# Kernel optimization log

Hardware: AMD Instinct MI355X
Metric: run time of the kernel (lower is better)

## Reference

```python
import jax, jax.numpy as jnp
import numpy as np

TEMPERATURE = 0.1
NEG_INF = -1e30  # finite sentinel to keep logsumexp grad-safe


def setup_inputs() -> dict:
    key = jax.random.key(0)
    k_emb, k_lab = jax.random.split(key)
    B, D, C = 8192, 256, 100
    embeddings = jax.random.normal(k_emb, (B, D), dtype=jnp.float32)
    labels = jax.random.randint(k_lab, (B,), 0, C, dtype=jnp.int64)
    return {"embeddings": embeddings, "labels": labels}


def reference(embeddings, labels):
    B = embeddings.shape[0]
    # squared L2 pairwise distance: ||x_i||^2 + ||x_j||^2 - 2 x_i . x_j
    sq = jnp.sum(embeddings * embeddings, axis=1)  # [B]
    gram = jnp.einsum('id,jd->ij', embeddings, embeddings)  # [B,B]
    dist2 = jnp.maximum(sq[:, None] + sq[None, :] - 2.0 * gram, 0.0)
    sim = -dist2 / TEMPERATURE  # [B,B]

    same = labels[:, None] == labels[None, :]
    eye = jnp.eye(B, dtype=bool)
    pos_mask = same & ~eye
    neg_mask = ~same

    # per-row uniform random positive via Gumbel-argmax over pos_mask
    k_sel = jax.random.key(42)
    g = jax.random.gumbel(k_sel, (B, B), dtype=jnp.float32)
    j = jnp.argmax(jnp.where(pos_mask, g, -jnp.inf), axis=1)  # [B]

    numerator = jnp.take_along_axis(sim, j[:, None], axis=1)[:, 0]  # sim[i, j_i]
    denominator = jax.nn.logsumexp(jnp.where(neg_mask, sim, NEG_INF), axis=1)

    valid = pos_mask.any(axis=1) & neg_mask.any(axis=1)
    per_row = -(numerator - denominator)
    n_valid = jnp.sum(valid)
    loss = jnp.sum(jnp.where(valid, per_row, 0.0)) / jnp.maximum(n_valid, 1)
    return jnp.where(n_valid > 0, loss, 0.0)
```

## Files before the change

### kernel.cpp

```cpp
#include <hip/hip_runtime.h>
#include <float.h>
#include <math.h>


#define B_N 8192
#define D_K 256
#define NCLS 100
#define MAXC 512
#define NSPLIT 16
#define NPART NSPLIT
#define JR (B_N / NSPLIT)
#define BI 128
#define BJ 64
#define NJT (JR / BJ)
#define BK 64
#define NKC (D_K / BK)
#define NEG_INF -1e30f
#define C2F  (-14.426950408889634f)
#define K2A  (28.853900817779268f)
#define LN2F (0.6931471805599453f)

typedef __attribute__((ext_vector_type(8))) short bf16x8;
typedef __attribute__((ext_vector_type(4))) float f32x4;
typedef unsigned short ushort_t;

__device__ __forceinline__ float ex2(float x){ return __builtin_amdgcn_exp2f(x); }
__device__ __forceinline__ float lg2(float x){ return __builtin_amdgcn_logf(x); }

__device__ __forceinline__ unsigned rotl32(unsigned x, int d){ return (x << d) | (x >> (32 - d)); }

__device__ __forceinline__ float gumbel_at(unsigned idx){
  const unsigned HALF = (unsigned)B_N * (unsigned)B_N / 2u;
  unsigned c0, c1; bool second;
  if (idx < HALF){ c0 = idx; c1 = idx + HALF; second = false; }
  else            { c0 = idx - HALF; c1 = idx; second = true; }
  const unsigned ks0 = 0u, ks1 = 42u, ks2 = 0u ^ 42u ^ 0x1BD11BDAu;
  unsigned x0 = c0 + ks0, x1 = c1 + ks1;
#define TF_RND(r) { x0 += x1; x1 = rotl32(x1, (r)); x1 ^= x0; }
  TF_RND(13) TF_RND(15) TF_RND(26) TF_RND(6)   x0 += ks1; x1 += ks2 + 1u;
  TF_RND(17) TF_RND(29) TF_RND(16) TF_RND(24)  x0 += ks2; x1 += ks0 + 2u;
  TF_RND(13) TF_RND(15) TF_RND(26) TF_RND(6)   x0 += ks0; x1 += ks1 + 3u;
  TF_RND(17) TF_RND(29) TF_RND(16) TF_RND(24)  x0 += ks1; x1 += ks2 + 4u;
  TF_RND(13) TF_RND(15) TF_RND(26) TF_RND(6)   x0 += ks2; x1 += ks0 + 5u;
#undef TF_RND
  unsigned bits = second ? x1 : x0;
  float u = __uint_as_float((bits >> 9) | 0x3f800000u) - 1.0f;
  const float TINY = 1.17549435e-38f;
  u = u * (1.0f - TINY) + TINY;
  u = fmaxf(TINY, u);
  return -logf(-logf(u));
}

__device__ __forceinline__ ushort_t f2bf(float x){
  unsigned u = __float_as_uint(x);
  return (ushort_t)((u + 0x7FFFu + ((u >> 16) & 1u)) >> 16);
}

__device__ __forceinline__ void async16(const ushort_t* g, ushort_t* lds_wave_base){
  __builtin_amdgcn_global_load_lds((const __attribute__((address_space(1))) void*)g,
                                   (__attribute__((address_space(3))) void*)lds_wave_base,
                                   16, 0, 0);
}

__global__ __launch_bounds__(256)
void prep_kernel(const float* __restrict__ E, ushort_t* __restrict__ Ebf,
                 float* __restrict__ sq, float* __restrict__ acc4,
                 const int* __restrict__ labels, int* __restrict__ cls_cnt,
                 int* __restrict__ clist){
  __shared__ int s_list[MAXC];
  __shared__ int s_n;
  if (blockIdx.x < B_N / 4){
    if (blockIdx.x == 0 && threadIdx.x < 4) acc4[threadIdx.x] = 0.f;
    int w = threadIdx.x >> 6, lane = threadIdx.x & 63;
    int row = blockIdx.x * 4 + w;
    const float4 v = *reinterpret_cast<const float4*>(E + (size_t)row * D_K + lane * 4);
    float s = v.x*v.x + v.y*v.y + v.z*v.z + v.w*v.w;
#pragma unroll
    for (int off = 32; off > 0; off >>= 1) s += __shfl_down(s, off);
    if (lane == 0) sq[row] = s;
    ushort4 o; o.x = f2bf(v.x); o.y = f2bf(v.y); o.z = f2bf(v.z); o.w = f2bf(v.w);
    *reinterpret_cast<ushort4*>(Ebf + (size_t)row * D_K + lane * 4) = o;
  } else {
    const int c = blockIdx.x - B_N / 4;
    const int tid = threadIdx.x;
    if (tid == 0) s_n = 0;
    __syncthreads();
    for (int t = tid; t < B_N; t += 256){
      if (labels[t] == c){
        int p = atomicAdd(&s_n, 1);
        if (p < MAXC) s_list[p] = t;
      }
    }
    __syncthreads();
    const int n = min(s_n, MAXC);
    if (tid == 0) cls_cnt[c] = n;
    for (int t = tid; t < n; t += 256) clist[c * MAXC + t] = s_list[t];
  }
}

__global__ __launch_bounds__(256)
void rowsel_kernel(const int* __restrict__ labels, const int* __restrict__ cls_cnt,
                   const int* __restrict__ clist, int* __restrict__ jsel){
  const int w = threadIdx.x >> 6, lane = threadIdx.x & 63;
  const int row = blockIdx.x * 4 + w;
  const int c = labels[row];
  const int n = min(cls_cnt[c], MAXC);
  float gb = -FLT_MAX; int jb = -1;
  for (int t = lane; t < n; t += 64){
    int j = clist[c * MAXC + t];
    if (j != row){
      float g = gumbel_at(((unsigned)row << 13) + (unsigned)j);
      if (g > gb || (g == gb && (unsigned)j < (unsigned)jb)){ gb = g; jb = j; }
    }
  }
#pragma unroll
  for (int off = 32; off > 0; off >>= 1){
    float g2 = __shfl_down(gb, off);
    int   j2 = __shfl_down(jb, off);
    if (g2 > gb || (g2 == gb && (unsigned)j2 < (unsigned)jb)){ gb = g2; jb = j2; }
  }
  if (lane == 0) jsel[row] = jb;
}

__global__ __launch_bounds__(256, 3)
void fused_kernel(const ushort_t* __restrict__ Ebf, const int* __restrict__ labels,
                  const float* __restrict__ sq, const int* __restrict__ jsel,
                  float* __restrict__ numer,
                  float* __restrict__ wsM, float* __restrict__ wsS)
{
  __shared__ __align__(16) ushort_t Bs[2][BJ * BK];
  __shared__ float s_h2j[JR];
  __shared__ int   s_lj[JR];
  __shared__ float s_h2i[BI];
  __shared__ int   s_li[BI];
  __shared__ int   s_ji[BI];

  const int bi    = blockIdx.x >> 4;
  const int split = blockIdx.x & 15;
  const int i0    = bi * BI;
  const int jbase = split * JR;
  const int tid   = threadIdx.x;
  const int lane  = tid & 63;
  const int w     = tid >> 6;
  const int quad  = lane >> 4;
  const int l15   = lane & 15;

  for (int t = tid; t < JR; t += 256){ s_h2j[t] = C2F * sq[jbase + t]; s_lj[t] = labels[jbase + t]; }
  if (tid < BI){ s_h2i[tid] = C2F * sq[i0 + tid]; s_li[tid] = labels[i0 + tid]; s_ji[tid] = jsel[i0 + tid]; }

  bf16x8 af[2][8];
#pragma unroll
  for (int mt = 0; mt < 2; mt++){
    const ushort_t* rp = Ebf + (size_t)(i0 + w * 32 + mt * 16 + l15) * D_K + quad * 8;
#pragma unroll
    for (int c = 0; c < 8; c++)
      af[mt][c] = *reinterpret_cast<const bf16x8*>(rp + c * 32);
  }

  f32x4 acc[2][4];
#pragma unroll
  for (int mt = 0; mt < 2; mt++)
#pragma unroll
    for (int nt = 0; nt < 4; nt++) acc[mt][nt] = (f32x4)0.f;
  float sm[8], ssum[8];
#pragma unroll
  for (int r = 0; r < 8; r++){ sm[r] = NEG_INF; ssum[r] = 0.f; }

  int soff[2];
#pragma unroll
  for (int rd = 0; rd < 2; rd++){
    int slot = rd * 256 + tid;
    int r = slot >> 3, gs = slot & 7;
    soff[rd] = r * D_K + ((gs ^ (r & 7)) << 3);
  }

#pragma unroll
  for (int rd = 0; rd < 2; rd++)
    async16(Ebf + (size_t)jbase * D_K + soff[rd],
            &Bs[0][(size_t)(rd * 256 + w * 64) * 8]);
  __syncthreads();

#pragma unroll 1
  for (int jt = 0; jt < NJT; jt++){
    const int j0 = jbase + jt * BJ;
#pragma unroll
    for (int kc = 0; kc < NKC; kc++){
      const int b = kc & 1;
      const int sn = jt * NKC + kc + 1;
      if (sn < NJT * NKC){
        const int kcn = sn & 3;
        const size_t gb0 = (size_t)(jbase + (sn >> 2) * BJ) * D_K + (size_t)kcn * BK;
#pragma unroll
        for (int rd = 0; rd < 2; rd++)
          async16(Ebf + gb0 + soff[rd],
                  &Bs[b ^ 1][(size_t)(rd * 256 + w * 64) * 8]);
      }
#pragma unroll
      for (int s = 0; s < 2; s++){
        const int g = s * 4 + quad;
        const int c = kc * 2 + s;
        bf16x8 bfr[4];
#pragma unroll
        for (int q = 0; q < 4; q++){
          int r = q * 16 + l15;
          bfr[q] = *reinterpret_cast<const bf16x8*>(&Bs[b][r * BK + ((g ^ (r & 7)) << 3)]);
        }
#pragma unroll
        for (int q = 0; q < 4; q++){
          acc[0][q] = __builtin_amdgcn_mfma_f32_16x16x32_bf16(af[0][c], bfr[q], acc[0][q], 0, 0, 0);
          acc[1][q] = __builtin_amdgcn_mfma_f32_16x16x32_bf16(af[1][c], bfr[q], acc[1][q], 0, 0, 0);
        }
      }
      if (kc == NKC - 1){
        float h2j[4]; int lj[4];
#pragma unroll
        for (int nt = 0; nt < 4; nt++){
          int ccol = jt * BJ + nt * 16 + l15;
          h2j[nt] = s_h2j[ccol]; lj[nt] = s_lj[ccol];
        }
#pragma unroll
        for (int mt = 0; mt < 2; mt++){
#pragma unroll
          for (int rr = 0; rr < 4; rr++){
            const int rl = w * 32 + mt * 16 + quad * 4 + rr;
            const float h2i = s_h2i[rl];
            const int lrow = s_li[rl], jsl = s_ji[rl];
            float sv[4];
#pragma unroll
            for (int nt = 0; nt < 4; nt++){
              float a = acc[mt][nt][rr];
              float sim2 = fminf(fmaf(K2A, a, h2i + h2j[nt]), 0.f);
              int colg = j0 + nt * 16 + l15;
              if (colg == jsl) numer[i0 + rl] = sim2;
              sv[nt] = (lj[nt] != lrow) ? sim2 : NEG_INF;
            }
            float m4 = fmaxf(fmaxf(sv[0], sv[1]), fmaxf(sv[2], sv[3]));
            float s4 = ex2(sv[0]-m4)+ex2(sv[1]-m4)+ex2(sv[2]-m4)+ex2(sv[3]-m4);
            const int sidx = mt * 4 + rr;
            float M = fmaxf(sm[sidx], m4);
            ssum[sidx] = ssum[sidx]*ex2(sm[sidx]-M) + s4*ex2(m4-M);
            sm[sidx] = M;
          }
        }
#pragma unroll
        for (int mt = 0; mt < 2; mt++)
#pragma unroll
          for (int nt = 0; nt < 4; nt++) acc[mt][nt] = (f32x4)0.f;
      }
      __syncthreads();
    }
  }

#pragma unroll
  for (int sidx = 0; sidx < 8; sidx++){
    float mv = sm[sidx], sv2 = ssum[sidx];
#pragma unroll
    for (int mask = 1; mask < 16; mask <<= 1){
      float m2 = __shfl_xor(mv, mask);
      float s2 = __shfl_xor(sv2, mask);
      float M = fmaxf(mv, m2);
      sv2 = sv2 * ex2(mv - M) + s2 * ex2(m2 - M);
      mv = M;
    }
    if (l15 == 0){
      const int mt = sidx >> 2, rr = sidx & 3;
      int rl = w * 32 + mt * 16 + quad * 4 + rr;
      int o = split * B_N + i0 + rl;
      wsM[o] = mv; wsS[o] = sv2;
    }
  }
}

__global__ __launch_bounds__(256)
void finale_kernel(const float* __restrict__ wsM, const float* __restrict__ wsS,
                   const float* __restrict__ numer, const int* __restrict__ jsel,
                   float* __restrict__ acc4, float* __restrict__ out)
{
  const int tid = threadIdx.x;
  const int row = blockIdx.x * 256 + tid;
  float M = -3.0e38f, S = 0.f;
#pragma unroll
  for (int p = 0; p < NPART; p++){
    float m2 = wsM[p * B_N + row], s2 = wsS[p * B_N + row];
    float Mn = fmaxf(M, m2);
    S = S * ex2(M - Mn) + s2 * ex2(m2 - Mn);
    M = Mn;
  }
  bool v = (jsel[row] >= 0) && (M > -5e29f);
  float s = v ? (LN2F * (M + lg2(S) - numer[row])) : 0.f;
  unsigned n = v ? 1u : 0u;
#pragma unroll
  for (int off = 32; off > 0; off >>= 1){ s += __shfl_down(s, off); n += __shfl_down(n, off); }
  __shared__ float ssm[4]; __shared__ unsigned snm[4];
  if ((tid & 63) == 0){ ssm[tid >> 6] = s; snm[tid >> 6] = n; }
  __syncthreads();
  if (tid == 0){
    float bs = ssm[0] + ssm[1] + ssm[2] + ssm[3];
    unsigned bn = snm[0] + snm[1] + snm[2] + snm[3];
    atomicAdd(&acc4[0], bs);
    atomicAdd((unsigned*)&acc4[1], bn);
    __threadfence();
    unsigned old = atomicAdd((unsigned*)&acc4[2], 1u);
    if (old == 31u){
      float St = atomicAdd(&acc4[0], 0.f);
      unsigned Nt = atomicAdd((unsigned*)&acc4[1], 0u);
      out[0] = (Nt > 0u) ? (St / (float)Nt) : 0.f;
    }
  }
}

extern "C" void kernel_launch(void* const* d_in, const int* in_sizes, int n_in,
                              void* d_out, int out_size, void* d_ws, size_t ws_size,
                              hipStream_t stream)
{
  const float* E      = (const float*)d_in[0];
  const int*   labels = (const int*)d_in[1];
  float*       out    = (float*)d_out;

  ushort_t* Ebf = (ushort_t*)d_ws;
  float* wsM    = (float*)(Ebf + (size_t)B_N * D_K);
  float* wsS    = wsM + NPART * B_N;
  float* sqb    = wsS + NPART * B_N;
  float* numer  = sqb + B_N;
  int* jsel     = (int*)(numer + B_N);
  float* acc4   = (float*)(jsel + B_N);
  int* cls_cnt  = (int*)(acc4 + 4);
  int* clist    = cls_cnt + NCLS;

  prep_kernel<<<B_N / 4 + NCLS, 256, 0, stream>>>(E, Ebf, sqb, acc4, labels, cls_cnt, clist);
  rowsel_kernel<<<B_N / 4, 256, 0, stream>>>(labels, cls_cnt, clist, jsel);
  fused_kernel<<<(B_N / BI) * NSPLIT, 256, 0, stream>>>(Ebf, labels, sqb, jsel, numer, wsM, wsS);
  finale_kernel<<<B_N / 256, 256, 0, stream>>>(wsM, wsS, numer, jsel, acc4, out);
}
```

Before: 145.5 us.

## Deepen LDS prefetch ring and fold positive selection into prep kernel

```diff
diff --git a/kernel.cpp b/kernel.cpp
--- a/kernel.cpp
+++ b/kernel.cpp
@@ -15,6 +15,8 @@
 #define NJT (JR / BJ)
 #define BK 64
 #define NKC (D_K / BK)
+#define NSTEP (NJT * NKC)
+#define TOTB ((B_N / BI) * NSPLIT)
 #define NEG_INF -1e30f
 #define C2F  (-14.426950408889634f)
 #define K2A  (28.853900817779268f)
@@ -65,8 +67,7 @@
 __global__ __launch_bounds__(256)
 void prep_kernel(const float* __restrict__ E, ushort_t* __restrict__ Ebf,
                  float* __restrict__ sq, float* __restrict__ acc4,
-                 const int* __restrict__ labels, int* __restrict__ cls_cnt,
-                 int* __restrict__ clist){
+                 const int* __restrict__ labels, int* __restrict__ jsel){
   __shared__ int s_list[MAXC];
   __shared__ int s_n;
   if (blockIdx.x < B_N / 4){
@@ -83,6 +84,7 @@
   } else {
     const int c = blockIdx.x - B_N / 4;
     const int tid = threadIdx.x;
+    const int w = tid >> 6, lane = tid & 63;
     if (tid == 0) s_n = 0;
     __syncthreads();
     for (int t = tid; t < B_N; t += 256){
@@ -93,42 +95,34 @@
     }
     __syncthreads();
     const int n = min(s_n, MAXC);
-    if (tid == 0) cls_cnt[c] = n;
-    for (int t = tid; t < n; t += 256) clist[c * MAXC + t] = s_list[t];
+    for (int m = w; m < n; m += 4){
+      const int row = s_list[m];
+      float gb = -FLT_MAX; int jb = -1;
+      for (int t = lane; t < n; t += 64){
+        int j = s_list[t];
+        if (j != row){
+          float g = gumbel_at(((unsigned)row << 13) + (unsigned)j);
+          if (g > gb || (g == gb && (unsigned)j < (unsigned)jb)){ gb = g; jb = j; }
+        }
+      }
+#pragma unroll
+      for (int off = 32; off > 0; off >>= 1){
+        float g2 = __shfl_down(gb, off);
+        int   j2 = __shfl_down(jb, off);
+        if (g2 > gb || (g2 == gb && (unsigned)j2 < (unsigned)jb)){ gb = g2; jb = j2; }
+      }
+      if (lane == 0) jsel[row] = jb;
+    }
   }
 }
 
 __global__ __launch_bounds__(256)
-void rowsel_kernel(const int* __restrict__ labels, const int* __restrict__ cls_cnt,
-                   const int* __restrict__ clist, int* __restrict__ jsel){
-  const int w = threadIdx.x >> 6, lane = threadIdx.x & 63;
-  const int row = blockIdx.x * 4 + w;
-  const int c = labels[row];
-  const int n = min(cls_cnt[c], MAXC);
-  float gb = -FLT_MAX; int jb = -1;
-  for (int t = lane; t < n; t += 64){
-    int j = clist[c * MAXC + t];
-    if (j != row){
-      float g = gumbel_at(((unsigned)row << 13) + (unsigned)j);
-      if (g > gb || (g == gb && (unsigned)j < (unsigned)jb)){ gb = g; jb = j; }
-    }
-  }
-#pragma unroll
-  for (int off = 32; off > 0; off >>= 1){
-    float g2 = __shfl_down(gb, off);
-    int   j2 = __shfl_down(jb, off);
-    if (g2 > gb || (g2 == gb && (unsigned)j2 < (unsigned)jb)){ gb = g2; jb = j2; }
-  }
-  if (lane == 0) jsel[row] = jb;
-}
-
-__global__ __launch_bounds__(256, 3)
 void fused_kernel(const ushort_t* __restrict__ Ebf, const int* __restrict__ labels,
                   const float* __restrict__ sq, const int* __restrict__ jsel,
                   float* __restrict__ numer,
                   float* __restrict__ wsM, float* __restrict__ wsS)
 {
-  __shared__ __align__(16) ushort_t Bs[2][BJ * BK];
+  __shared__ __align__(16) ushort_t Bs[4][BJ * BK];
   __shared__ float s_h2j[JR];
   __shared__ int   s_lj[JR];
   __shared__ float s_h2i[BI];
@@ -148,24 +142,6 @@
   for (int t = tid; t < JR; t += 256){ s_h2j[t] = C2F * sq[jbase + t]; s_lj[t] = labels[jbase + t]; }
   if (tid < BI){ s_h2i[tid] = C2F * sq[i0 + tid]; s_li[tid] = labels[i0 + tid]; s_ji[tid] = jsel[i0 + tid]; }
 
-  bf16x8 af[2][8];
-#pragma unroll
-  for (int mt = 0; mt < 2; mt++){
-    const ushort_t* rp = Ebf + (size_t)(i0 + w * 32 + mt * 16 + l15) * D_K + quad * 8;
-#pragma unroll
-    for (int c = 0; c < 8; c++)
-      af[mt][c] = *reinterpret_cast<const bf16x8*>(rp + c * 32);
-  }
-
-  f32x4 acc[2][4];
-#pragma unroll
-  for (int mt = 0; mt < 2; mt++)
-#pragma unroll
-    for (int nt = 0; nt < 4; nt++) acc[mt][nt] = (f32x4)0.f;
-  float sm[8], ssum[8];
-#pragma unroll
-  for (int r = 0; r < 8; r++){ sm[r] = NEG_INF; ssum[r] = 0.f; }
-
   int soff[2];
 #pragma unroll
   for (int rd = 0; rd < 2; rd++){
@@ -175,9 +151,30 @@
   }
 
 #pragma unroll
-  for (int rd = 0; rd < 2; rd++)
-    async16(Ebf + (size_t)jbase * D_K + soff[rd],
-            &Bs[0][(size_t)(rd * 256 + w * 64) * 8]);
+  for (int st = 0; st < 2; st++)
+#pragma unroll
+    for (int rd = 0; rd < 2; rd++)
+      async16(Ebf + (size_t)jbase * D_K + (size_t)st * BK + soff[rd],
+              &Bs[st][(size_t)(rd * 256 + w * 64) * 8]);
+
+  bf16x8 af[2][8];
+#pragma unroll
+  for (int mt = 0; mt < 2; mt++){
+    const ushort_t* rp = Ebf + (size_t)(i0 + w * 32 + mt * 16 + l15) * D_K + quad * 8;
+#pragma unroll
+    for (int c = 0; c < 8; c++)
+      af[mt][c] = *reinterpret_cast<const bf16x8*>(rp + c * 32);
+  }
+
+  f32x4 acc[2][4];
+#pragma unroll
+  for (int mt = 0; mt < 2; mt++)
+#pragma unroll
+    for (int nt = 0; nt < 4; nt++) acc[mt][nt] = (f32x4)0.f;
+  float sm[8], ssum[8];
+#pragma unroll
+  for (int r = 0; r < 8; r++){ sm[r] = NEG_INF; ssum[r] = 0.f; }
+
   __syncthreads();
 
 #pragma unroll 1
@@ -185,32 +182,33 @@
     const int j0 = jbase + jt * BJ;
 #pragma unroll
     for (int kc = 0; kc < NKC; kc++){
-      const int b = kc & 1;
-      const int sn = jt * NKC + kc + 1;
-      if (sn < NJT * NKC){
-        const int kcn = sn & 3;
-        const size_t gb0 = (size_t)(jbase + (sn >> 2) * BJ) * D_K + (size_t)kcn * BK;
+      const int st = jt * NKC + kc;
+      if (st <= NSTEP - 3){
+        const int sn = st + 2;
+        const size_t gb0 = (size_t)(jbase + (sn >> 2) * BJ) * D_K + (size_t)(sn & 3) * BK;
 #pragma unroll
         for (int rd = 0; rd < 2; rd++)
-          async16(Ebf + gb0 + soff[rd],
-                  &Bs[b ^ 1][(size_t)(rd * 256 + w * 64) * 8]);
-      }
+          async16(Ebf + gb0 + soff[rd], &Bs[sn & 3][(size_t)(rd * 256 + w * 64) * 8]);
+        asm volatile("s_waitcnt vmcnt(4)\n\ts_barrier" ::: "memory");
+      } else if (st == NSTEP - 2){
+        asm volatile("s_waitcnt vmcnt(2)\n\ts_barrier" ::: "memory");
+      } else {
+        asm volatile("s_waitcnt vmcnt(0)\n\ts_barrier" ::: "memory");
+      }
+      __builtin_amdgcn_s_setprio(1);
 #pragma unroll
       for (int s = 0; s < 2; s++){
         const int g = s * 4 + quad;
         const int c = kc * 2 + s;
-        bf16x8 bfr[4];
 #pragma unroll
         for (int q = 0; q < 4; q++){
-          int r = q * 16 + l15;
-          bfr[q] = *reinterpret_cast<const bf16x8*>(&Bs[b][r * BK + ((g ^ (r & 7)) << 3)]);
+          const int r = q * 16 + l15;
+          bf16x8 bq = *reinterpret_cast<const bf16x8*>(&Bs[kc][r * BK + ((g ^ (r & 7)) << 3)]);
+          acc[0][q] = __builtin_amdgcn_mfma_f32_16x16x32_bf16(af[0][c], bq, acc[0][q], 0, 0, 0);
+          acc[1][q] = __builtin_amdgcn_mfma_f32_16x16x32_bf16(af[1][c], bq, acc[1][q], 0, 0, 0);
         }
-#pragma unroll
-        for (int q = 0; q < 4; q++){
-          acc[0][q] = __builtin_amdgcn_mfma_f32_16x16x32_bf16(af[0][c], bfr[q], acc[0][q], 0, 0, 0);
-          acc[1][q] = __builtin_amdgcn_mfma_f32_16x16x32_bf16(af[1][c], bfr[q], acc[1][q], 0, 0, 0);
-        }
-      }
+      }
+      __builtin_amdgcn_s_setprio(0);
       if (kc == NKC - 1){
         float h2j[4]; int lj[4];
 #pragma unroll
@@ -247,7 +245,6 @@
 #pragma unroll
           for (int nt = 0; nt < 4; nt++) acc[mt][nt] = (f32x4)0.f;
       }
-      __syncthreads();
     }
   }
 
@@ -324,11 +321,8 @@
   float* numer  = sqb + B_N;
   int* jsel     = (int*)(numer + B_N);
   float* acc4   = (float*)(jsel + B_N);
-  int* cls_cnt  = (int*)(acc4 + 4);
-  int* clist    = cls_cnt + NCLS;
-
-  prep_kernel<<<B_N / 4 + NCLS, 256, 0, stream>>>(E, Ebf, sqb, acc4, labels, cls_cnt, clist);
-  rowsel_kernel<<<B_N / 4, 256, 0, stream>>>(labels, cls_cnt, clist, jsel);
-  fused_kernel<<<(B_N / BI) * NSPLIT, 256, 0, stream>>>(Ebf, labels, sqb, jsel, numer, wsM, wsS);
+
+  prep_kernel<<<B_N / 4 + NCLS, 256, 0, stream>>>(E, Ebf, sqb, acc4, labels, jsel);
+  fused_kernel<<<TOTB, 256, 0, stream>>>(Ebf, labels, sqb, jsel, numer, wsM, wsS);
   finale_kernel<<<B_N / 256, 256, 0, stream>>>(wsM, wsS, numer, jsel, acc4, out);
 }
```

New measurement: 179.8 us. 1.24x slower.

## Load full-K B tile per j-tile instead of double-buffered K chunks

Applied to the files above, without the earlier changes.

```diff
diff --git a/kernel.cpp b/kernel.cpp
--- a/kernel.cpp
+++ b/kernel.cpp
@@ -13,8 +13,7 @@
 #define BI 128
 #define BJ 64
 #define NJT (JR / BJ)
-#define BK 64
-#define NKC (D_K / BK)
+#define TOTB ((B_N / BI) * NSPLIT)
 #define NEG_INF -1e30f
 #define C2F  (-14.426950408889634f)
 #define K2A  (28.853900817779268f)
@@ -122,13 +121,13 @@
   if (lane == 0) jsel[row] = jb;
 }
 
-__global__ __launch_bounds__(256, 3)
+__global__ __launch_bounds__(256)
 void fused_kernel(const ushort_t* __restrict__ Ebf, const int* __restrict__ labels,
                   const float* __restrict__ sq, const int* __restrict__ jsel,
                   float* __restrict__ numer,
                   float* __restrict__ wsM, float* __restrict__ wsS)
 {
-  __shared__ __align__(16) ushort_t Bs[2][BJ * BK];
+  __shared__ __align__(16) ushort_t Bs[BJ * D_K];
   __shared__ float s_h2j[JR];
   __shared__ int   s_lj[JR];
   __shared__ float s_h2i[BI];
@@ -166,89 +165,74 @@
 #pragma unroll
   for (int r = 0; r < 8; r++){ sm[r] = NEG_INF; ssum[r] = 0.f; }
 
-  int soff[2];
-#pragma unroll
-  for (int rd = 0; rd < 2; rd++){
-    int slot = rd * 256 + tid;
-    int r = slot >> 3, gs = slot & 7;
-    soff[rd] = r * D_K + ((gs ^ (r & 7)) << 3);
-  }
-
-#pragma unroll
-  for (int rd = 0; rd < 2; rd++)
-    async16(Ebf + (size_t)jbase * D_K + soff[rd],
-            &Bs[0][(size_t)(rd * 256 + w * 64) * 8]);
+  const int soff0 = (tid >> 5) * D_K + (((tid & 31) ^ ((tid >> 5) & 7)) << 3);
+
   __syncthreads();
 
 #pragma unroll 1
   for (int jt = 0; jt < NJT; jt++){
     const int j0 = jbase + jt * BJ;
-#pragma unroll
-    for (int kc = 0; kc < NKC; kc++){
-      const int b = kc & 1;
-      const int sn = jt * NKC + kc + 1;
-      if (sn < NJT * NKC){
-        const int kcn = sn & 3;
-        const size_t gb0 = (size_t)(jbase + (sn >> 2) * BJ) * D_K + (size_t)kcn * BK;
-#pragma unroll
-        for (int rd = 0; rd < 2; rd++)
-          async16(Ebf + gb0 + soff[rd],
-                  &Bs[b ^ 1][(size_t)(rd * 256 + w * 64) * 8]);
-      }
-#pragma unroll
-      for (int s = 0; s < 2; s++){
-        const int g = s * 4 + quad;
-        const int c = kc * 2 + s;
-        bf16x8 bfr[4];
-#pragma unroll
-        for (int q = 0; q < 4; q++){
-          int r = q * 16 + l15;
-          bfr[q] = *reinterpret_cast<const bf16x8*>(&Bs[b][r * BK + ((g ^ (r & 7)) << 3)]);
+    const ushort_t* gsrc = Ebf + (size_t)j0 * D_K + soff0;
+#pragma unroll
+    for (int rd = 0; rd < 8; rd++)
+      async16(gsrc + rd * (8 * D_K), &Bs[(size_t)(rd * 256 + w * 64) * 8]);
+    __syncthreads();
+
+    __builtin_amdgcn_s_setprio(1);
+#pragma unroll
+    for (int c = 0; c < 8; c++){
+      const int g = c * 4 + quad;
+      bf16x8 bq[4];
+#pragma unroll
+      for (int q = 0; q < 4; q++){
+        const int r = q * 16 + l15;
+        bq[q] = *reinterpret_cast<const bf16x8*>(&Bs[r * D_K + ((g ^ (r & 7)) << 3)]);
+      }
+#pragma unroll
+      for (int q = 0; q < 4; q++){
+        acc[0][q] = __builtin_amdgcn_mfma_f32_16x16x32_bf16(af[0][c], bq[q], acc[0][q], 0, 0, 0);
+        acc[1][q] = __builtin_amdgcn_mfma_f32_16x16x32_bf16(af[1][c], bq[q], acc[1][q], 0, 0, 0);
+      }
+    }
+    __builtin_amdgcn_s_setprio(0);
+
+    {
+      float h2j[4]; int lj[4];
+#pragma unroll
+      for (int nt = 0; nt < 4; nt++){
+        int ccol = jt * BJ + nt * 16 + l15;
+        h2j[nt] = s_h2j[ccol]; lj[nt] = s_lj[ccol];
+      }
+#pragma unroll
+      for (int mt = 0; mt < 2; mt++){
+#pragma unroll
+        for (int rr = 0; rr < 4; rr++){
+          const int rl = w * 32 + mt * 16 + quad * 4 + rr;
+          const float h2i = s_h2i[rl];
+          const int lrow = s_li[rl], jsl = s_ji[rl];
+          float sv[4];
+#pragma unroll
+          for (int nt = 0; nt < 4; nt++){
+            float a = acc[mt][nt][rr];
+            float sim2 = fminf(fmaf(K2A, a, h2i + h2j[nt]), 0.f);
+            int colg = j0 + nt * 16 + l15;
+            if (colg == jsl) numer[i0 + rl] = sim2;
+            sv[nt] = (lj[nt] != lrow) ? sim2 : NEG_INF;
+          }
+          float m4 = fmaxf(fmaxf(sv[0], sv[1]), fmaxf(sv[2], sv[3]));
+          float s4 = ex2(sv[0]-m4)+ex2(sv[1]-m4)+ex2(sv[2]-m4)+ex2(sv[3]-m4);
+          const int sidx = mt * 4 + rr;
+          float M = fmaxf(sm[sidx], m4);
+          ssum[sidx] = ssum[sidx]*ex2(sm[sidx]-M) + s4*ex2(m4-M);
+          sm[sidx] = M;
         }
-#pragma unroll
-        for (int q = 0; q < 4; q++){
-          acc[0][q] = __builtin_amdgcn_mfma_f32_16x16x32_bf16(af[0][c], bfr[q], acc[0][q], 0, 0, 0);
-          acc[1][q] = __builtin_amdgcn_mfma_f32_16x16x32_bf16(af[1][c], bfr[q], acc[1][q], 0, 0, 0);
-        }
-      }
-      if (kc == NKC - 1){
-        float h2j[4]; int lj[4];
-#pragma unroll
-        for (int nt = 0; nt < 4; nt++){
-          int ccol = jt * BJ + nt * 16 + l15;
-          h2j[nt] = s_h2j[ccol]; lj[nt] = s_lj[ccol];
-        }
-#pragma unroll
-        for (int mt = 0; mt < 2; mt++){
-#pragma unroll
-          for (int rr = 0; rr < 4; rr++){
-            const int rl = w * 32 + mt * 16 + quad * 4 + rr;
-            const float h2i = s_h2i[rl];
-            const int lrow = s_li[rl], jsl = s_ji[rl];
-            float sv[4];
-#pragma unroll
-            for (int nt = 0; nt < 4; nt++){
-              float a = acc[mt][nt][rr];
-              float sim2 = fminf(fmaf(K2A, a, h2i + h2j[nt]), 0.f);
-              int colg = j0 + nt * 16 + l15;
-              if (colg == jsl) numer[i0 + rl] = sim2;
-              sv[nt] = (lj[nt] != lrow) ? sim2 : NEG_INF;
-            }
-            float m4 = fmaxf(fmaxf(sv[0], sv[1]), fmaxf(sv[2], sv[3]));
-            float s4 = ex2(sv[0]-m4)+ex2(sv[1]-m4)+ex2(sv[2]-m4)+ex2(sv[3]-m4);
-            const int sidx = mt * 4 + rr;
-            float M = fmaxf(sm[sidx], m4);
-            ssum[sidx] = ssum[sidx]*ex2(sm[sidx]-M) + s4*ex2(m4-M);
-            sm[sidx] = M;
-          }
-        }
-#pragma unroll
-        for (int mt = 0; mt < 2; mt++)
-#pragma unroll
-          for (int nt = 0; nt < 4; nt++) acc[mt][nt] = (f32x4)0.f;
-      }
-      __syncthreads();
-    }
+      }
+#pragma unroll
+      for (int mt = 0; mt < 2; mt++)
+#pragma unroll
+        for (int nt = 0; nt < 4; nt++) acc[mt][nt] = (f32x4)0.f;
+    }
+    __syncthreads();
   }
 
 #pragma unroll
@@ -329,6 +313,6 @@
 
   prep_kernel<<<B_N / 4 + NCLS, 256, 0, stream>>>(E, Ebf, sqb, acc4, labels, cls_cnt, clist);
   rowsel_kernel<<<B_N / 4, 256, 0, stream>>>(labels, cls_cnt, clist, jsel);
-  fused_kernel<<<(B_N / BI) * NSPLIT, 256, 0, stream>>>(Ebf, labels, sqb, jsel, numer, wsM, wsS);
+  fused_kernel<<<TOTB, 256, 0, stream>>>(Ebf, labels, sqb, jsel, numer, wsM, wsS);
   finale_kernel<<<B_N / 256, 256, 0, stream>>>(wsM, wsS, numer, jsel, acc4, out);
 }
```

Result: faster. 139.8 us (-3.9%).
